# Kernel tuning notes

Measured on AMD Instinct MI355X. Metric: run time of the kernel, lower is better.

## Reference

```python
import jax, jax.numpy as jnp
import numpy as np

EMBED_DIM = 1024
NUM_HEADS = 16
HEAD_DIM = EMBED_DIM // NUM_HEADS
B, N = 4, 2048


def setup_inputs() -> dict:
    key = jax.random.key(0)
    ks = jax.random.split(key, 12)
    s = 1.0 / np.sqrt(EMBED_DIM)
    inp = {
        "x": jax.random.normal(ks[0], (B, N, EMBED_DIM), dtype=jnp.float32),
        "dist_matrix": jax.random.uniform(ks[1], (N, N), dtype=jnp.float32),
        # Linear weights stored torch-style [out, in]
        "Wq": jax.random.normal(ks[2], (EMBED_DIM, EMBED_DIM), dtype=jnp.float32) * s,
        "bq": jnp.zeros((EMBED_DIM,), dtype=jnp.float32),
        "Wk": jax.random.normal(ks[3], (EMBED_DIM, EMBED_DIM), dtype=jnp.float32) * s,
        "bk": jnp.zeros((EMBED_DIM,), dtype=jnp.float32),
        "Wv": jax.random.normal(ks[4], (EMBED_DIM, EMBED_DIM), dtype=jnp.float32) * s,
        "bv": jnp.zeros((EMBED_DIM,), dtype=jnp.float32),
        "Wo": jax.random.normal(ks[5], (EMBED_DIM, EMBED_DIM), dtype=jnp.float32) * s,
        "bo": jnp.zeros((EMBED_DIM,), dtype=jnp.float32),
        # DistanceBias params: bias = dist_w * dist + dist_b (learned scalar affine)
        "dist_w": jnp.asarray(-1.0, dtype=jnp.float32),
        "dist_b": jnp.asarray(0.0, dtype=jnp.float32),
    }
    return inp


def reference(x, dist_matrix, Wq, bq, Wk, bk, Wv, bv, Wo, bo, dist_w, dist_b):
    b, n, c = x.shape
    h, d = NUM_HEADS, HEAD_DIM
    # projections (torch Linear: x @ W.T + b), reshape to [b, h, n, d]
    def proj(W, bias):
        y = jnp.einsum('bnc,oc->bno', x, W) + bias
        return y.reshape(b, n, h, d).transpose(0, 2, 1, 3)
    q = proj(Wq, bq)
    k = proj(Wk, bk)
    v = proj(Wv, bv)
    scores = jnp.einsum('bhnd,bhmd->bhnm', q, k) / np.sqrt(d).astype(np.float32)
    bias = dist_w * dist_matrix + dist_b            # [N, N], shared over b, h
    scores = scores + bias[None, None, :, :]
    attn = jax.nn.softmax(scores, axis=-1)
    out = jnp.einsum('bhnm,bhmd->bhnd', attn, v)    # [b, h, n, d]
    out = out.transpose(0, 2, 1, 3).reshape(b, n, c)
    return jnp.einsum('bnc,oc->bno', out, Wo) + bo
```

## Files before the change

### kernel.cpp

```cpp
#include <hip/hip_runtime.h>
#include <stdint.h>

typedef unsigned short ushort;
typedef __attribute__((ext_vector_type(8))) short bf16x8;
typedef __attribute__((ext_vector_type(4))) float f32x4;
typedef __attribute__((ext_vector_type(16))) float f32x16;

__device__ __forceinline__ float b2f(ushort u) {
    return __uint_as_float(((unsigned)u) << 16);
}
__device__ __forceinline__ ushort f2b(float f) {
    unsigned u = __float_as_uint(f);
    u += 0x7fff + ((u >> 16) & 1);
    return (ushort)(u >> 16);
}

#if __has_builtin(__builtin_amdgcn_exp2f)
#define EXP2(x) __builtin_amdgcn_exp2f(x)
#else
#define EXP2(x) __expf((x) * 0.69314718056f)
#endif

__device__ __forceinline__ unsigned cvtpk(float a, float b) {
    unsigned r;
    asm("v_cvt_pk_bf16_f32 %0, %1, %2" : "=v"(r) : "v"(a), "v"(b));
    return r;
}

__device__ __forceinline__ void plswap(unsigned &a, unsigned &b) {
#if __has_builtin(__builtin_amdgcn_permlane32_swap)
    auto r = __builtin_amdgcn_permlane32_swap(a, b, 0, 0);
    a = (unsigned)r[0]; b = (unsigned)r[1];
#else
    asm volatile("v_permlane32_swap_b32 %0, %1" : "+v"(a), "+v"(b));
#endif
}

#define SEQN 2048
#define EMB  1024
#define NH   16
#define HD   64
#define BHSTRIDE (SEQN * HD)

__device__ __forceinline__ void gload16(const ushort* g, ushort* l) {
    __builtin_amdgcn_global_load_lds(
        (const __attribute__((address_space(1))) unsigned int*)g,
        (__attribute__((address_space(3))) unsigned int*)l, 16, 0, 0);
}

__global__ __launch_bounds__(256) void conv_x(
        const float* __restrict__ s, ushort* __restrict__ d) {
    const size_t i = (size_t)blockIdx.x * 256 + threadIdx.x;
    float4 a = ((const float4*)s)[2 * i];
    float4 b = ((const float4*)s)[2 * i + 1];
    ushort pk[8] = {f2b(a.x), f2b(a.y), f2b(a.z), f2b(a.w),
                    f2b(b.x), f2b(b.y), f2b(b.z), f2b(b.w)};
    ((uint4*)d)[i] = *(uint4*)pk;
}

__global__ __launch_bounds__(256) void conv_w4(
        const float* __restrict__ W0, const float* __restrict__ W1,
        const float* __restrict__ W2, const float* __restrict__ W3,
        ushort* __restrict__ d) {
    const float* s = (blockIdx.y == 0) ? W0 : (blockIdx.y == 1) ? W1
                   : (blockIdx.y == 2) ? W2 : W3;
    ushort* dst = d + ((size_t)blockIdx.y << 20);
    const size_t i = (size_t)blockIdx.x * 256 + threadIdx.x;
    float4 a = ((const float4*)s)[2 * i];
    float4 b = ((const float4*)s)[2 * i + 1];
    ushort pk[8] = {f2b(a.x), f2b(a.y), f2b(a.z), f2b(a.w),
                    f2b(b.x), f2b(b.y), f2b(b.z), f2b(b.w)};
    ((uint4*)dst)[i] = *(uint4*)pk;
}

__global__ __launch_bounds__(256) void conv_Lp(
        const float* __restrict__ dist, const float* __restrict__ dw,
        const float* __restrict__ db, float* __restrict__ Lp) {
    const float c1 = dw[0] * 1.44269504f, c2 = db[0] * 1.44269504f;
    const size_t gid = (size_t)blockIdx.x * 256 + threadIdx.x;
    const int lo  = (int)(gid & 31);
    const int kv4 = (int)((gid >> 5) & 511);
    const int qt  = (int)(gid >> 14);
    const int q   = qt * 32 + lo;
    float4 d = *(const float4*)(dist + (size_t)q * SEQN + kv4 * 4);
    float4 o = {fmaf(d.x, c1, c2), fmaf(d.y, c1, c2),
                fmaf(d.z, c1, c2), fmaf(d.w, c1, c2)};
    ((float4*)Lp)[gid] = o;
}

#define LDSZ (128 * 32)

__global__ __launch_bounds__(256) void gemm_qkv(
        const ushort* __restrict__ xb, const ushort* __restrict__ Wb,
        const float* __restrict__ bq, const float* __restrict__ bk,
        const float* __restrict__ bv,
        ushort* __restrict__ qb, ushort* __restrict__ kb,
        ushort* __restrict__ vT) {
    __shared__ ushort As[LDSZ];
    __shared__ ushort Bs[LDSZ];
    const int m0   = blockIdx.x * 128;
    const int nt   = blockIdx.y;
    const int wsel = nt >> 3;
    const int n0   = (nt & 7) * 128;
    const ushort* W    = Wb + ((size_t)wsel << 20);
    const float* bias  = (wsel == 0) ? bq : (wsel == 1) ? bk : bv;

    const int t = threadIdx.x, lane = t & 63, wave = t >> 6;
    const int ln = lane & 15, quad = lane >> 4;
    const int wm = wave & 1, wn = wave >> 1;

    const int e0 = wave * 128 + lane;
    const int e1 = e0 + 64;
    const ushort* gA0 = xb + (size_t)(m0 + (e0 >> 2)) * 1024 + (e0 & 3) * 8;
    const ushort* gA1 = xb + (size_t)(m0 + (e1 >> 2)) * 1024 + (e1 & 3) * 8;
    const ushort* gB0 = W  + (size_t)(n0 + (e0 >> 2)) * 1024 + (e0 & 3) * 8;
    const ushort* gB1 = W  + (size_t)(n0 + (e1 >> 2)) * 1024 + (e1 & 3) * 8;
    ushort* lA0 = As + wave * 1024;
    ushort* lA1 = lA0 + 512;
    ushort* lB0 = Bs + wave * 1024;
    ushort* lB1 = lB0 + 512;

    f32x4 acc[4][4];
#pragma unroll
    for (int i = 0; i < 4; i++)
#pragma unroll
        for (int j = 0; j < 4; j++) acc[i][j] = (f32x4){0.f, 0.f, 0.f, 0.f};

    for (int k0 = 0; k0 < 1024; k0 += 32) {
        __syncthreads();
        gload16(gA0 + k0, lA0);
        gload16(gA1 + k0, lA1);
        gload16(gB0 + k0, lB0);
        gload16(gB1 + k0, lB1);
        __syncthreads();
        bf16x8 af[4], bfr[4];
#pragma unroll
        for (int i = 0; i < 4; i++)
            af[i]  = *(bf16x8*)&As[(wm * 64 + i * 16 + ln) * 32 + quad * 8];
#pragma unroll
        for (int j = 0; j < 4; j++)
            bfr[j] = *(bf16x8*)&Bs[(wn * 64 + j * 16 + ln) * 32 + quad * 8];
#pragma unroll
        for (int i = 0; i < 4; i++)
#pragma unroll
            for (int j = 0; j < 4; j++)
                acc[i][j] = __builtin_amdgcn_mfma_f32_16x16x32_bf16(
                                af[i], bfr[j], acc[i][j], 0, 0, 0);
    }

    if (wsel < 2) {
        ushort* dst = (wsel == 0) ? qb : kb;
        const float scale = (wsel == 0) ? 0.125f : 1.0f;
#pragma unroll
        for (int j = 0; j < 4; j++) {
            const int o  = n0 + wn * 64 + j * 16 + ln;
            const float bval = bias[o];
            const int h = o >> 6, d = o & 63;
#pragma unroll
            for (int i = 0; i < 4; i++) {
                const int mg = m0 + wm * 64 + i * 16 + quad * 4;
#pragma unroll
                for (int r = 0; r < 4; r++) {
                    const int m  = mg + r;
                    const int b  = m >> 11;
                    const int ns = m & 2047;
                    dst[(size_t)(b * NH + h) * BHSTRIDE + (size_t)ns * HD + d] =
                        f2b((acc[i][j][r] + bval) * scale);
                }
            }
        }
    } else {
#pragma unroll
        for (int j = 0; j < 4; j++) {
            const int o  = n0 + wn * 64 + j * 16 + ln;
            const float bval = bias[o];
            const int h = o >> 6, d = o & 63;
#pragma unroll
            for (int i = 0; i < 4; i++) {
                const int mg = m0 + wm * 64 + i * 16 + quad * 4;
                const int b  = mg >> 11;
                const int ns = mg & 2047;
                ushort pk[4];
#pragma unroll
                for (int r = 0; r < 4; r++) pk[r] = f2b(acc[i][j][r] + bval);
                *(uint2*)&vT[(size_t)(b * NH + h) * BHSTRIDE +
                             (size_t)d * SEQN + ns] = *(uint2*)&pk[0];
            }
        }
    }
}

__global__ __launch_bounds__(256) void attn(
        ushort* q,
        const ushort* __restrict__ k,
        const ushort* __restrict__ vT,
        const float* __restrict__ Lp) {
    __shared__ short Ks[64 * 72];
    __shared__ short Vs[64 * 72];
    const int t = threadIdx.x, lane = t & 63, wave = t >> 6;
    const int lo = lane & 31, hi = lane >> 5;
    const int h = blockIdx.y, b = blockIdx.z;
    const int bh = b * NH + h;
    const int qw0 = blockIdx.x * 128 + wave * 32;

    ushort* qp = q + (size_t)bh * BHSTRIDE;
    const ushort* kp = k  + (size_t)bh * BHSTRIDE;
    const ushort* vp = vT + (size_t)bh * BHSTRIDE;
    const float4* Lp4 = (const float4*)Lp + ((size_t)(qw0 >> 5) * 512) * 32 + lo;

    const int sr = t >> 2;
    const int sc = (t & 3) * 16;

    bf16x8 qf[4];
#pragma unroll
    for (int kk = 0; kk < 4; kk++)
        qf[kk] = *(const bf16x8*)(qp + (size_t)(qw0 + lo) * HD + kk * 16 + hi * 8);

    f32x16 O[2];
#pragma unroll
    for (int dt = 0; dt < 2; dt++)
#pragma unroll
        for (int i = 0; i < 16; i++) O[dt][i] = 0.f;
    float lsum = 0.f;

    uint4 krg0 = *(const uint4*)(kp + (size_t)sr * HD + sc);
    uint4 krg1 = *(const uint4*)(kp + (size_t)sr * HD + sc + 8);
    uint4 vrg0 = *(const uint4*)(vp + (size_t)sr * SEQN + sc);
    uint4 vrg1 = *(const uint4*)(vp + (size_t)sr * SEQN + sc + 8);

    for (int kt = 0; kt < 32; kt++) {
        const int kv0 = kt * 64;
        __syncthreads();
        *(uint4*)&Ks[sr * 72 + sc]     = krg0;
        *(uint4*)&Ks[sr * 72 + sc + 8] = krg1;
        *(uint4*)&Vs[sr * 72 + sc]     = vrg0;
        *(uint4*)&Vs[sr * 72 + sc + 8] = vrg1;
        __syncthreads();
        const int kvn = (kv0 + 64) & 2047;
        krg0 = *(const uint4*)(kp + (size_t)(kvn + sr) * HD + sc);
        krg1 = *(const uint4*)(kp + (size_t)(kvn + sr) * HD + sc + 8);
        vrg0 = *(const uint4*)(vp + (size_t)sr * SEQN + kvn + sc);
        vrg1 = *(const uint4*)(vp + (size_t)sr * SEQN + kvn + sc + 8);

#pragma unroll
        for (int s = 0; s < 2; s++) {
            f32x16 z;
#pragma unroll
            for (int i = 0; i < 16; i++) z[i] = 0.f;
#pragma unroll
            for (int kk = 0; kk < 4; kk++) {
                bf16x8 kf = *(bf16x8*)&Ks[(s * 32 + lo) * 72 + kk * 16 + hi * 8];
                z = __builtin_amdgcn_mfma_f32_32x32x16_bf16(kf, qf[kk], z, 0, 0, 0);
            }
            float p[16];
#pragma unroll
            for (int n = 0; n < 4; n++) {
                float4 lv = Lp4[((kv0 >> 2) + s * 8 + hi + 2 * n) * 32];
#pragma unroll
                for (int m = 0; m < 4; m++) {
                    float pv = EXP2(fmaf(z[n * 4 + m], 1.44269504f,
                                         ((const float*)&lv)[m]));
                    lsum += pv;
                    p[n * 4 + m] = pv;
                }
            }
#pragma unroll
            for (int kl = 0; kl < 2; kl++) {
                unsigned a0 = cvtpk(p[kl * 8 + 0], p[kl * 8 + 1]);
                unsigned b0 = cvtpk(p[kl * 8 + 4], p[kl * 8 + 5]);
                plswap(a0, b0);
                unsigned a1 = cvtpk(p[kl * 8 + 2], p[kl * 8 + 3]);
                unsigned b1 = cvtpk(p[kl * 8 + 6], p[kl * 8 + 7]);
                plswap(a1, b1);
                union { bf16x8 v; unsigned u[4]; } pf;
                pf.u[0] = a0; pf.u[1] = a1; pf.u[2] = b0; pf.u[3] = b1;
                const int kvk = s * 2 + kl;
#pragma unroll
                for (int dt = 0; dt < 2; dt++) {
                    bf16x8 vf = *(bf16x8*)&Vs[(dt * 32 + lo) * 72 +
                                              kvk * 16 + hi * 8];
                    O[dt] = __builtin_amdgcn_mfma_f32_32x32x16_bf16(
                                vf, pf.v, O[dt], 0, 0, 0);
                }
            }
        }
    }

    float tot = lsum + __shfl_xor(lsum, 32);
    const float inv = 1.0f / tot;
#pragma unroll
    for (int dt = 0; dt < 2; dt++)
#pragma unroll
        for (int n = 0; n < 4; n++) {
            uint2 pk2;
            pk2.x = cvtpk(O[dt][n * 4 + 0] * inv, O[dt][n * 4 + 1] * inv);
            pk2.y = cvtpk(O[dt][n * 4 + 2] * inv, O[dt][n * 4 + 3] * inv);
            *(uint2*)(qp + (size_t)(qw0 + lo) * HD + dt * 32 + hi * 4 + n * 8)
                = pk2;
        }
}

__global__ __launch_bounds__(256) void gemm_out(
        const ushort* __restrict__ ao, const ushort* __restrict__ Wob,
        const float* __restrict__ bias, float* __restrict__ out) {
    __shared__ ushort As[LDSZ];
    __shared__ ushort Bs[LDSZ];
    const int m0 = blockIdx.x * 128;
    const int n0 = blockIdx.y * 128;
    const int t = threadIdx.x, lane = t & 63, wave = t >> 6;
    const int ln = lane & 15, quad = lane >> 4;
    const int wm = wave & 1, wn = wave >> 1;

    const int e0 = wave * 128 + lane;
    const int e1 = e0 + 64;
    const int bb = m0 >> 11;
    const int nbase = m0 & 2047;
    const ushort* gA0 = ao + ((size_t)bb << 21) +
                        (size_t)(nbase + (e0 >> 2)) * 64 + (e0 & 3) * 8;
    const ushort* gA1 = ao + ((size_t)bb << 21) +
                        (size_t)(nbase + (e1 >> 2)) * 64 + (e1 & 3) * 8;
    const ushort* gB0 = Wob + (size_t)(n0 + (e0 >> 2)) * 1024 + (e0 & 3) * 8;
    const ushort* gB1 = Wob + (size_t)(n0 + (e1 >> 2)) * 1024 + (e1 & 3) * 8;
    ushort* lA0 = As + wave * 1024;
    ushort* lA1 = lA0 + 512;
    ushort* lB0 = Bs + wave * 1024;
    ushort* lB1 = lB0 + 512;

    f32x4 acc[4][4];
#pragma unroll
    for (int i = 0; i < 4; i++)
#pragma unroll
        for (int j = 0; j < 4; j++) acc[i][j] = (f32x4){0.f, 0.f, 0.f, 0.f};

    for (int k0 = 0; k0 < 1024; k0 += 32) {
        const size_t aoff = ((size_t)(k0 >> 6) << 17) + (k0 & 32);
        __syncthreads();
        gload16(gA0 + aoff, lA0);
        gload16(gA1 + aoff, lA1);
        gload16(gB0 + k0, lB0);
        gload16(gB1 + k0, lB1);
        __syncthreads();
        bf16x8 af[4], bfr[4];
#pragma unroll
        for (int i = 0; i < 4; i++)
            af[i]  = *(bf16x8*)&As[(wm * 64 + i * 16 + ln) * 32 + quad * 8];
#pragma unroll
        for (int j = 0; j < 4; j++)
            bfr[j] = *(bf16x8*)&Bs[(wn * 64 + j * 16 + ln) * 32 + quad * 8];
#pragma unroll
        for (int i = 0; i < 4; i++)
#pragma unroll
            for (int j = 0; j < 4; j++)
                acc[i][j] = __builtin_amdgcn_mfma_f32_16x16x32_bf16(
                                af[i], bfr[j], acc[i][j], 0, 0, 0);
    }

#pragma unroll
    for (int j = 0; j < 4; j++) {
        const int o = n0 + wn * 64 + j * 16 + ln;
        const float bval = bias[o];
#pragma unroll
        for (int i = 0; i < 4; i++) {
            const int mg = m0 + wm * 64 + i * 16 + quad * 4;
#pragma unroll
            for (int r = 0; r < 4; r++)
                out[(size_t)(mg + r) * EMB + o] = acc[i][j][r] + bval;
        }
    }
}

extern "C" void kernel_launch(void* const* d_in, const int* in_sizes, int n_in,
                              void* d_out, int out_size, void* d_ws, size_t ws_size,
                              hipStream_t stream) {
    const float* x    = (const float*)d_in[0];
    const float* dist = (const float*)d_in[1];
    const float* Wq   = (const float*)d_in[2];
    const float* bq   = (const float*)d_in[3];
    const float* Wk   = (const float*)d_in[4];
    const float* bk   = (const float*)d_in[5];
    const float* Wv   = (const float*)d_in[6];
    const float* bv   = (const float*)d_in[7];
    const float* Wo   = (const float*)d_in[8];
    const float* bo   = (const float*)d_in[9];
    const float* dw   = (const float*)d_in[10];
    const float* db   = (const float*)d_in[11];

    const size_t PLANE = (size_t)8192 * 1024;
    ushort* qb = (ushort*)d_ws;
    ushort* kb = qb + PLANE;
    ushort* xb = kb + PLANE;
    ushort* Wb = xb + PLANE;
    ushort* vT = (ushort*)d_out;
    float*  Lf = (float*)(vT + PLANE);

    dim3 blk(256);
    conv_x       <<<dim3(4096),      blk, 0, stream>>>(x, xb);
    conv_w4      <<<dim3(512, 4),    blk, 0, stream>>>(Wq, Wk, Wv, Wo, Wb);
    conv_Lp      <<<dim3(4096),      blk, 0, stream>>>(dist, dw, db, Lf);
    gemm_qkv     <<<dim3(64, 24),    blk, 0, stream>>>(xb, Wb, bq, bk, bv,
                                                       qb, kb, vT);
    attn         <<<dim3(16, 16, 4), blk, 0, stream>>>(qb, kb, vT, Lf);
    gemm_out     <<<dim3(64, 8),     blk, 0, stream>>>(qb, Wb + 3 * (size_t)(1 << 20),
                                                       bo, (float*)d_out);
}
```

Measured before the change: 344.4 us.

## Double-buffer K/V shared tiles in attention and prefetch distance-bias loads

Shared-memory K/V tiles become double-buffered, so each iteration writes the next tile into the alternate buffer and needs one barrier per step instead of two. The register prefetch now runs two tiles ahead. All distance-bias loads for a tile are issued up front, and s_setprio raises wave priority around the MFMA sections. Launch bounds request 4 blocks per CU, which caps registers and may cause spills, and shared memory per block doubles.

```diff
diff --git a/kernel.cpp b/kernel.cpp
--- a/kernel.cpp
+++ b/kernel.cpp
@@ -190,13 +190,13 @@
     }
 }
 
-__global__ __launch_bounds__(256) void attn(
+__global__ __launch_bounds__(256, 4) void attn(
         ushort* q,
         const ushort* __restrict__ k,
         const ushort* __restrict__ vT,
         const float* __restrict__ Lp) {
-    __shared__ short Ks[64 * 72];
-    __shared__ short Vs[64 * 72];
+    __shared__ short Ks[2][64 * 72];
+    __shared__ short Vs[2][64 * 72];
     const int t = threadIdx.x, lane = t & 63, wave = t >> 6;
     const int lo = lane & 31, hi = lane >> 5;
     const int h = blockIdx.y, b = blockIdx.z;
@@ -227,39 +227,54 @@
     uint4 krg1 = *(const uint4*)(kp + (size_t)sr * HD + sc + 8);
     uint4 vrg0 = *(const uint4*)(vp + (size_t)sr * SEQN + sc);
     uint4 vrg1 = *(const uint4*)(vp + (size_t)sr * SEQN + sc + 8);
+    *(uint4*)&Ks[0][sr * 72 + sc]     = krg0;
+    *(uint4*)&Ks[0][sr * 72 + sc + 8] = krg1;
+    *(uint4*)&Vs[0][sr * 72 + sc]     = vrg0;
+    *(uint4*)&Vs[0][sr * 72 + sc + 8] = vrg1;
+    krg0 = *(const uint4*)(kp + (size_t)(64 + sr) * HD + sc);
+    krg1 = *(const uint4*)(kp + (size_t)(64 + sr) * HD + sc + 8);
+    vrg0 = *(const uint4*)(vp + (size_t)sr * SEQN + 64 + sc);
+    vrg1 = *(const uint4*)(vp + (size_t)sr * SEQN + 64 + sc + 8);
 
     for (int kt = 0; kt < 32; kt++) {
         const int kv0 = kt * 64;
+        const int cb = kt & 1;
         __syncthreads();
-        *(uint4*)&Ks[sr * 72 + sc]     = krg0;
-        *(uint4*)&Ks[sr * 72 + sc + 8] = krg1;
-        *(uint4*)&Vs[sr * 72 + sc]     = vrg0;
-        *(uint4*)&Vs[sr * 72 + sc + 8] = vrg1;
-        __syncthreads();
-        const int kvn = (kv0 + 64) & 2047;
+        *(uint4*)&Ks[cb ^ 1][sr * 72 + sc]     = krg0;
+        *(uint4*)&Ks[cb ^ 1][sr * 72 + sc + 8] = krg1;
+        *(uint4*)&Vs[cb ^ 1][sr * 72 + sc]     = vrg0;
+        *(uint4*)&Vs[cb ^ 1][sr * 72 + sc + 8] = vrg1;
+        const int kvn = (kv0 + 128) & 2047;
         krg0 = *(const uint4*)(kp + (size_t)(kvn + sr) * HD + sc);
         krg1 = *(const uint4*)(kp + (size_t)(kvn + sr) * HD + sc + 8);
         vrg0 = *(const uint4*)(vp + (size_t)sr * SEQN + kvn + sc);
         vrg1 = *(const uint4*)(vp + (size_t)sr * SEQN + kvn + sc + 8);
+        float4 lv2[2][4];
+#pragma unroll
+        for (int s = 0; s < 2; s++)
+#pragma unroll
+            for (int n = 0; n < 4; n++)
+                lv2[s][n] = Lp4[((kv0 >> 2) + s * 8 + hi + 2 * n) * 32];
 
 #pragma unroll
         for (int s = 0; s < 2; s++) {
             f32x16 z;
 #pragma unroll
             for (int i = 0; i < 16; i++) z[i] = 0.f;
+            __builtin_amdgcn_s_setprio(1);
 #pragma unroll
             for (int kk = 0; kk < 4; kk++) {
-                bf16x8 kf = *(bf16x8*)&Ks[(s * 32 + lo) * 72 + kk * 16 + hi * 8];
+                bf16x8 kf = *(bf16x8*)&Ks[cb][(s * 32 + lo) * 72 + kk * 16 + hi * 8];
                 z = __builtin_amdgcn_mfma_f32_32x32x16_bf16(kf, qf[kk], z, 0, 0, 0);
             }
+            __builtin_amdgcn_s_setprio(0);
             float p[16];
 #pragma unroll
             for (int n = 0; n < 4; n++) {
-                float4 lv = Lp4[((kv0 >> 2) + s * 8 + hi + 2 * n) * 32];
 #pragma unroll
                 for (int m = 0; m < 4; m++) {
                     float pv = EXP2(fmaf(z[n * 4 + m], 1.44269504f,
-                                         ((const float*)&lv)[m]));
+                                         ((const float*)&lv2[s][n])[m]));
                     lsum += pv;
                     p[n * 4 + m] = pv;
                 }
@@ -275,13 +290,15 @@
                 union { bf16x8 v; unsigned u[4]; } pf;
                 pf.u[0] = a0; pf.u[1] = a1; pf.u[2] = b0; pf.u[3] = b1;
                 const int kvk = s * 2 + kl;
+                __builtin_amdgcn_s_setprio(1);
 #pragma unroll
                 for (int dt = 0; dt < 2; dt++) {
-                    bf16x8 vf = *(bf16x8*)&Vs[(dt * 32 + lo) * 72 +
-                                              kvk * 16 + hi * 8];
+                    bf16x8 vf = *(bf16x8*)&Vs[cb][(dt * 32 + lo) * 72 +
+                                                  kvk * 16 + hi * 8];
                     O[dt] = __builtin_amdgcn_mfma_f32_32x32x16_bf16(
                                 vf, pf.v, O[dt], 0, 0, 0);
                 }
+                __builtin_amdgcn_s_setprio(0);
             }
         }
     }
```

New measurement: 322.5 us. 6.4% less time.
